# Kernel tuning notes

Measured on AMD Instinct MI355X. Metric: run time of the kernel, lower is better.

## Reference

```python
import jax, jax.numpy as jnp
import numpy as np
import math

B, N, IN_DIM, OUT_DIM, H = 8, 1024, 256, 256, 8
D_K = OUT_DIM // H


def setup_inputs() -> dict:
    key = jax.random.key(0)
    ks = jax.random.split(key, 12)
    s_in = 1.0 / math.sqrt(IN_DIM)
    s_out = 1.0 / math.sqrt(OUT_DIM)
    return {
        "X": jax.random.normal(ks[0], (B, N, IN_DIM), jnp.float32),
        "A": jax.random.randint(ks[1], (B, N, N), 0, 2, jnp.int32),
        "D": jax.random.uniform(ks[2], (B, N, N), jnp.float32),
        "W_q": jax.random.uniform(ks[3], (IN_DIM, OUT_DIM), jnp.float32, -s_in, s_in),
        "b_q": jax.random.uniform(ks[4], (OUT_DIM,), jnp.float32, -s_in, s_in),
        "W_k": jax.random.uniform(ks[5], (IN_DIM, OUT_DIM), jnp.float32, -s_in, s_in),
        "b_k": jax.random.uniform(ks[6], (OUT_DIM,), jnp.float32, -s_in, s_in),
        "W_v": jax.random.uniform(ks[7], (IN_DIM, OUT_DIM), jnp.float32, -s_in, s_in),
        "b_v": jax.random.uniform(ks[8], (OUT_DIM,), jnp.float32, -s_in, s_in),
        "W_o": jax.random.uniform(ks[9], (OUT_DIM, OUT_DIM), jnp.float32, -s_out, s_out),
        "b_o": jax.random.uniform(ks[10], (OUT_DIM,), jnp.float32, -s_out, s_out),
        "dist_scale": jnp.array(1.0, jnp.float32),
    }


def reference(X, A, D, W_q, b_q, W_k, b_k, W_v, b_v, W_o, b_o, dist_scale):
    b, n, _ = X.shape
    # Projections -> [B, H, N, d_k]
    Q = (X @ W_q + b_q).reshape(b, n, H, D_K).transpose(0, 2, 1, 3)
    K = (X @ W_k + b_k).reshape(b, n, H, D_K).transpose(0, 2, 1, 3)
    V = (X @ W_v + b_v).reshape(b, n, H, D_K).transpose(0, 2, 1, 3)
    scores = jnp.einsum("bhqd,bhkd->bhqk", Q, K) / jnp.sqrt(jnp.float32(D_K))
    scores = scores - dist_scale * D[:, None, :, :]
    scores = jnp.where(A[:, None, :, :] <= 0, jnp.float32(-1e9), scores)
    attn = jax.nn.softmax(scores, axis=-1)  # dropout is identity in eval mode
    out = jnp.einsum("bhqk,bhkd->bhqd", attn, V)
    out = out.transpose(0, 2, 1, 3).reshape(b, n, H * D_K)
    return out @ W_o + b_o
```

## Files before the change

kernel.cpp:

```cpp
#include <hip/hip_runtime.h>


typedef _Float16 f16x8 __attribute__((ext_vector_type(8)));
typedef __fp16 h16x2 __attribute__((ext_vector_type(2)));
typedef float f32x4 __attribute__((ext_vector_type(4)));
typedef int i32x4 __attribute__((ext_vector_type(4)));
typedef unsigned short u16x8 __attribute__((ext_vector_type(8)));

#define DEV static __device__ __forceinline__

#define LOG2E 1.4426950408889634f
#define QSCALE 0.2550351062f

DEV unsigned short f2h(float f) {
  _Float16 h = (_Float16)f;
  unsigned short u;
  __builtin_memcpy(&u, &h, 2);
  return u;
}

DEV f32x4 mfma16h(f16x8 a, f16x8 b, f32x4 c) {
  return __builtin_amdgcn_mfma_f32_16x16x32_f16(a, b, c, 0, 0, 0);
}

DEV f16x8 ldfragh(const unsigned short* p) {
  return *reinterpret_cast<const f16x8*>(p);
}

__global__ __launch_bounds__(256) void k_prep_xw(
    const float* __restrict__ X,
    const float* __restrict__ Wq, const float* __restrict__ Wk,
    const float* __restrict__ Wv, const float* __restrict__ Wo,
    unsigned short* __restrict__ Xh, unsigned short* __restrict__ Wt) {
  const int tid = blockIdx.x * 256 + threadIdx.x;
  const int NX4 = (8192 * 256) / 4;
  if (tid < NX4) {
    float4 v = reinterpret_cast<const float4*>(X)[tid];
    union { h16x2 h2[2]; ushort4 u; } o;
    o.h2[0] = __builtin_amdgcn_cvt_pkrtz(v.x, v.y);
    o.h2[1] = __builtin_amdgcn_cvt_pkrtz(v.z, v.w);
    reinterpret_cast<ushort4*>(Xh)[tid] = o.u;
  } else {
    int t = tid - NX4;
    int mat = t >> 16;
    int e = t & 65535;
    int n = e >> 8, k = e & 255;
    const float* W = (mat == 0) ? Wq : (mat == 1) ? Wk : (mat == 2) ? Wv : Wo;
    Wt[t] = f2h(W[k * 256 + n]);
  }
}

__global__ __launch_bounds__(256, 2) void k_qkv_bias(
    const unsigned short* __restrict__ Xh, const unsigned short* __restrict__ Wt,
    const float* __restrict__ bq, const float* __restrict__ bk,
    const float* __restrict__ bv,
    const int* __restrict__ A, const float* __restrict__ D,
    const float* __restrict__ dscale,
    unsigned short* __restrict__ Qb, unsigned short* __restrict__ Kb,
    unsigned short* __restrict__ Vt, unsigned short* __restrict__ Bias) {
  if (blockIdx.x >= 384) {
    const int t = (blockIdx.x - 384) * 256 + threadIdx.x;
    const i32x4 a4 = reinterpret_cast<const i32x4*>(A)[t];
    const f32x4 d4 = reinterpret_cast<const f32x4*>(D)[t];
    const float c = -dscale[0] * LOG2E;
    ushort4 o;
    unsigned short* op = (unsigned short*)&o;
    #pragma unroll
    for (int i = 0; i < 4; ++i)
      op[i] = f2h(a4[i] <= 0 ? -60000.0f : c * d4[i]);
    reinterpret_cast<ushort4*>(Bias)[t] = o;
    return;
  }

  const int lane = threadIdx.x & 63;
  const int w = threadIdx.x >> 6;
  const int lr = lane & 15, lg = lane >> 4;
  const int yy = blockIdx.x >> 5;
  const int mat = yy >> 2;
  const int nloc = (yy & 3) * 64 + w * 16;
  const int mbase = (blockIdx.x & 31) << 8;

  const unsigned short* Wm = Wt + mat * 65536;
  const float* bias = (mat == 0) ? bq : (mat == 1) ? bk : bv;

  f16x8 bfr[8];
  #pragma unroll
  for (int ks = 0; ks < 8; ++ks)
    bfr[ks] = ldfragh(Wm + (nloc + lr) * 256 + ks * 32 + lg * 8);
  const float bb = bias[nloc + lr];
  const int cm = nloc + lr;
  const int hh = cm >> 5, d = cm & 31;

  for (int mt = 0; mt < 16; ++mt) {
    const int m0 = mbase + mt * 16;
    f16x8 a[8];
    #pragma unroll
    for (int ks = 0; ks < 8; ++ks)
      a[ks] = ldfragh(Xh + (m0 + lr) * 256 + ks * 32 + lg * 8);
    f32x4 acc = {0.f, 0.f, 0.f, 0.f};
    #pragma unroll
    for (int ks = 0; ks < 8; ++ks)
      acc = mfma16h(a[ks], bfr[ks], acc);

    if (mat == 2) {
      union { h16x2 h2[2]; ushort4 u; } vv;
      vv.h2[0] = __builtin_amdgcn_cvt_pkrtz(acc[0] + bb, acc[1] + bb);
      vv.h2[1] = __builtin_amdgcn_cvt_pkrtz(acc[2] + bb, acc[3] + bb);
      const int row = m0 + lg * 4;
      const int bidx = row >> 10, nn = row & 1023;
      *reinterpret_cast<ushort4*>(&Vt[(((bidx * 8 + hh) * 32) + d) * 1024 + nn]) = vv.u;
    } else if (mat == 0) {
      #pragma unroll
      for (int i = 0; i < 4; ++i) {
        const int row = m0 + lg * 4 + i;
        const int bidx = row >> 10, nn = row & 1023;
        Qb[(((bidx * 8 + hh) * 1024) + nn) * 32 + d] = f2h((acc[i] + bb) * QSCALE);
      }
    } else {
      #pragma unroll
      for (int i = 0; i < 4; ++i) {
        const int row = m0 + lg * 4 + i;
        const int bidx = row >> 10, nn = row & 1023;
        Kb[(((bidx * 8 + hh) * 1024) + nn) * 32 + d] = f2h(acc[i] + bb);
      }
    }
  }
}

__global__ __launch_bounds__(512, 2) void k_attn(
    const unsigned short* __restrict__ Qb, const unsigned short* __restrict__ Kb,
    const unsigned short* __restrict__ Vt, const unsigned short* __restrict__ Bias,
    unsigned short* __restrict__ AO) {
  __shared__ alignas(16) unsigned short Klds[1024 * 32];
  __shared__ alignas(16) unsigned short Vlds[32 * 1024];
  __shared__ alignas(16) unsigned short Sbuf[8][2][16][40];

  const int tid = threadIdx.x;
  const int lane = tid & 63;
  const int w = tid >> 6;
  const int lr = lane & 15, lg = lane >> 4;
  const int bi = blockIdx.x;
  const int b = bi & 7;
  const int j = bi >> 3;
  const int h = j >> 2, qq = j & 3;
  const int q0w = qq * 256 + w * 32;

  const unsigned short* Kg = Kb + ((size_t)(b * 8 + h) << 15);
  const unsigned short* Vg = Vt + ((size_t)(b * 8 + h) << 15);
  const unsigned short* Qh = Qb + ((size_t)(b * 8 + h) << 15);

  #pragma unroll
  for (int p = 0; p < 8; ++p) {
    const int c = tid + p * 512;
    const int row = c >> 2, seg = c & 3;
    const u16x8 v = *reinterpret_cast<const u16x8*>(Kg + c * 8);
    *reinterpret_cast<u16x8*>(&Klds[row * 32 + ((seg ^ (row & 3)) << 3)]) = v;
  }
  #pragma unroll
  for (int p = 0; p < 8; ++p) {
    const int c = tid + p * 512;
    const int row = c >> 7, ch = c & 127;
    const u16x8 v = *reinterpret_cast<const u16x8*>(Vg + c * 8);
    *reinterpret_cast<u16x8*>(&Vlds[row * 1024 + ((ch ^ (row & 7)) << 3)]) = v;
  }

  f16x8 qf[2];
  qf[0] = ldfragh(Qh + (q0w + lr) * 32 + lg * 8);
  qf[1] = ldfragh(Qh + (q0w + 16 + lr) * 32 + lg * 8);
  const unsigned short* Br0 = Bias + ((size_t)b << 20) + (size_t)(q0w + lr) * 1024;
  const unsigned short* Br1 = Br0 + (size_t)16 * 1024;

  u16x8 bc[2][2], bn[2][2];
  #pragma unroll
  for (int hf = 0; hf < 2; ++hf) {
    bc[0][hf] = *reinterpret_cast<const u16x8*>(Br0 + hf * 32 + lg * 8);
    bc[1][hf] = *reinterpret_cast<const u16x8*>(Br1 + hf * 32 + lg * 8);
  }

  __syncthreads();

  f32x4 o[2][2];
  f32x4 lacc[2];
  #pragma unroll
  for (int s = 0; s < 2; ++s) {
    #pragma unroll
    for (int dh = 0; dh < 2; ++dh) o[s][dh] = f32x4{0.f, 0.f, 0.f, 0.f};
    lacc[s] = f32x4{0.f, 0.f, 0.f, 0.f};
  }
  f16x8 onesv;
  #pragma unroll
  for (int i = 0; i < 8; ++i) onesv[i] = (_Float16)1.0f;

  for (int t = 0; t < 16; ++t) {
    const int k0 = t << 6;
    if (t < 15) {
      #pragma unroll
      for (int hf = 0; hf < 2; ++hf) {
        bn[0][hf] = *reinterpret_cast<const u16x8*>(Br0 + k0 + 64 + hf * 32 + lg * 8);
        bn[1][hf] = *reinterpret_cast<const u16x8*>(Br1 + k0 + 64 + hf * 32 + lg * 8);
      }
    }

    f16x8 kf[4];
    #pragma unroll
    for (int st = 0; st < 4; ++st) {
      const int row = k0 + st * 16 + lr;
      kf[st] = *reinterpret_cast<const f16x8*>(
          &Klds[row * 32 + ((lg ^ (lr & 3)) << 3)]);
    }
    f16x8 vf[2][2];
    #pragma unroll
    for (int dh = 0; dh < 2; ++dh)
      #pragma unroll
      for (int hf = 0; hf < 2; ++hf) {
        const int row = dh * 16 + lr;
        const int ch = t * 8 + ((hf * 4 + lg) ^ (lr & 7));
        vf[dh][hf] = *reinterpret_cast<const f16x8*>(&Vlds[row * 1024 + ch * 8]);
      }

    #pragma unroll
    for (int hf = 0; hf < 2; ++hf) {
      const f32x4 zz = {0.f, 0.f, 0.f, 0.f};
      f32x4 sv[2][2];
      #pragma unroll
      for (int s = 0; s < 2; ++s)
        #pragma unroll
        for (int st = 0; st < 2; ++st)
          sv[s][st] = mfma16h(kf[hf * 2 + st], qf[s], zz);

      #pragma unroll
      for (int s = 0; s < 2; ++s)
        #pragma unroll
        for (int st = 0; st < 2; ++st) {
          union { h16x2 h2[2]; ushort4 u; } sw;
          sw.h2[0] = __builtin_amdgcn_cvt_pkrtz(sv[s][st][0], sv[s][st][1]);
          sw.h2[1] = __builtin_amdgcn_cvt_pkrtz(sv[s][st][2], sv[s][st][3]);
          *reinterpret_cast<ushort4*>(&Sbuf[w][s][lr][st * 16 + lg * 4]) = sw.u;
        }

      #pragma unroll
      for (int s = 0; s < 2; ++s) {
        const f16x8 sf = *reinterpret_cast<const f16x8*>(&Sbuf[w][s][lr][lg * 8]);
        const f16x8 bfv = *reinterpret_cast<const f16x8*>(&bc[s][hf]);
        const f16x8 sb = sf + bfv;
        float e[8];
        #pragma unroll
        for (int i = 0; i < 8; ++i) e[i] = exp2f((float)sb[i]);
        union { h16x2 h2[4]; f16x8 v; } pfu;
        #pragma unroll
        for (int i = 0; i < 4; ++i)
          pfu.h2[i] = __builtin_amdgcn_cvt_pkrtz(e[2 * i], e[2 * i + 1]);
        const f16x8 pf = pfu.v;
        o[s][0] = mfma16h(vf[0][hf], pf, o[s][0]);
        o[s][1] = mfma16h(vf[1][hf], pf, o[s][1]);
        lacc[s] = mfma16h(onesv, pf, lacc[s]);
      }
    }

    #pragma unroll
    for (int s = 0; s < 2; ++s)
      #pragma unroll
      for (int hf = 0; hf < 2; ++hf)
        bc[s][hf] = bn[s][hf];
  }

  #pragma unroll
  for (int s = 0; s < 2; ++s) {
    const float linv = 1.0f / lacc[s][0];
    ushort4 r0, r1;
    unsigned short* r0p = (unsigned short*)&r0;
    unsigned short* r1p = (unsigned short*)&r1;
    #pragma unroll
    for (int i = 0; i < 4; ++i) {
      r0p[i] = f2h(o[s][0][i] * linv);
      r1p[i] = f2h(o[s][1][i] * linv);
    }
    const int row = (b << 10) + q0w + s * 16 + lr;
    *reinterpret_cast<ushort4*>(&AO[row * 256 + h * 32 + lg * 4]) = r0;
    *reinterpret_cast<ushort4*>(&AO[row * 256 + h * 32 + 16 + lg * 4]) = r1;
  }
}

__global__ __launch_bounds__(256, 2) void k_oproj(
    const unsigned short* __restrict__ AO, const unsigned short* __restrict__ Wto,
    const float* __restrict__ bo, float* __restrict__ out) {
  const int lane = threadIdx.x & 63;
  const int w = threadIdx.x >> 6;
  const int lr = lane & 15, lg = lane >> 4;
  const int c0 = blockIdx.y * 64 + w * 16;
  const int mbase = blockIdx.x << 7;

  f16x8 bfr[8];
  #pragma unroll
  for (int ks = 0; ks < 8; ++ks)
    bfr[ks] = ldfragh(Wto + (c0 + lr) * 256 + ks * 32 + lg * 8);
  const float bb = bo[c0 + lr];

  for (int mt = 0; mt < 8; ++mt) {
    const int m0 = mbase + mt * 16;
    f16x8 a[8];
    #pragma unroll
    for (int ks = 0; ks < 8; ++ks)
      a[ks] = ldfragh(AO + (m0 + lr) * 256 + ks * 32 + lg * 8);
    f32x4 acc = {0.f, 0.f, 0.f, 0.f};
    #pragma unroll
    for (int ks = 0; ks < 8; ++ks)
      acc = mfma16h(a[ks], bfr[ks], acc);
    #pragma unroll
    for (int i = 0; i < 4; ++i) {
      const int row = m0 + lg * 4 + i;
      out[row * 256 + c0 + lr] = acc[i] + bb;
    }
  }
}

extern "C" void kernel_launch(void* const* d_in, const int* in_sizes, int n_in,
                              void* d_out, int out_size, void* d_ws, size_t ws_size,
                              hipStream_t stream) {
  const float* X   = (const float*)d_in[0];
  const int*   A   = (const int*)d_in[1];
  const float* D   = (const float*)d_in[2];
  const float* Wq  = (const float*)d_in[3];
  const float* bq  = (const float*)d_in[4];
  const float* Wk  = (const float*)d_in[5];
  const float* bk  = (const float*)d_in[6];
  const float* Wv  = (const float*)d_in[7];
  const float* bv  = (const float*)d_in[8];
  const float* Wo  = (const float*)d_in[9];
  const float* bo  = (const float*)d_in[10];
  const float* dsc = (const float*)d_in[11];
  float* out = (float*)d_out;

  unsigned short* ws = (unsigned short*)d_ws;
  unsigned short* Xh   = ws;
  unsigned short* Wt   = ws + 2097152;
  unsigned short* Qb   = ws + 2359296;
  unsigned short* Kb   = ws + 4456448;
  unsigned short* Vt   = ws + 6553600;
  unsigned short* Bias = ws + 8650752;
  unsigned short* AO   = Xh;

  hipLaunchKernelGGL(k_prep_xw, dim3(3072), dim3(256), 0, stream,
                     X, Wq, Wk, Wv, Wo, Xh, Wt);
  hipLaunchKernelGGL(k_qkv_bias, dim3(8576), dim3(256), 0, stream,
                     Xh, Wt, bq, bk, bv, A, D, dsc, Qb, Kb, Vt, Bias);
  hipLaunchKernelGGL(k_attn, dim3(256), dim3(512), 0, stream,
                     Qb, Kb, Vt, Bias, AO);
  hipLaunchKernelGGL(k_oproj, dim3(64, 4), dim3(256), 0, stream,
                     AO, Wt + 196608, bo, out);
}
```

Baseline: 84.80 us.

## Fuse adjacency mask and distance bias into attention kernel, drop bias precompute

New measurement: 120.7 us. 1.42x slower.

```diff
diff --git a/kernel.cpp b/kernel.cpp
--- a/kernel.cpp
+++ b/kernel.cpp
@@ -50,28 +50,12 @@
   }
 }
 
-__global__ __launch_bounds__(256, 2) void k_qkv_bias(
+__global__ __launch_bounds__(256, 2) void k_qkv(
     const unsigned short* __restrict__ Xh, const unsigned short* __restrict__ Wt,
     const float* __restrict__ bq, const float* __restrict__ bk,
     const float* __restrict__ bv,
-    const int* __restrict__ A, const float* __restrict__ D,
-    const float* __restrict__ dscale,
     unsigned short* __restrict__ Qb, unsigned short* __restrict__ Kb,
-    unsigned short* __restrict__ Vt, unsigned short* __restrict__ Bias) {
-  if (blockIdx.x >= 384) {
-    const int t = (blockIdx.x - 384) * 256 + threadIdx.x;
-    const i32x4 a4 = reinterpret_cast<const i32x4*>(A)[t];
-    const f32x4 d4 = reinterpret_cast<const f32x4*>(D)[t];
-    const float c = -dscale[0] * LOG2E;
-    ushort4 o;
-    unsigned short* op = (unsigned short*)&o;
-    #pragma unroll
-    for (int i = 0; i < 4; ++i)
-      op[i] = f2h(a4[i] <= 0 ? -60000.0f : c * d4[i]);
-    reinterpret_cast<ushort4*>(Bias)[t] = o;
-    return;
-  }
-
+    unsigned short* __restrict__ Vt) {
   const int lane = threadIdx.x & 63;
   const int w = threadIdx.x >> 6;
   const int lr = lane & 15, lg = lane >> 4;
@@ -129,7 +113,8 @@
 
 __global__ __launch_bounds__(512, 2) void k_attn(
     const unsigned short* __restrict__ Qb, const unsigned short* __restrict__ Kb,
-    const unsigned short* __restrict__ Vt, const unsigned short* __restrict__ Bias,
+    const unsigned short* __restrict__ Vt, const int* __restrict__ A,
+    const float* __restrict__ D, const float* __restrict__ dsc,
     unsigned short* __restrict__ AO) {
   __shared__ alignas(16) unsigned short Klds[1024 * 32];
   __shared__ alignas(16) unsigned short Vlds[32 * 1024];
@@ -144,6 +129,7 @@
   const int j = bi >> 3;
   const int h = j >> 2, qq = j & 3;
   const int q0w = qq * 256 + w * 32;
+  const float c = -dsc[0] * LOG2E;
 
   const unsigned short* Kg = Kb + ((size_t)(b * 8 + h) << 15);
   const unsigned short* Vg = Vt + ((size_t)(b * 8 + h) << 15);
@@ -151,31 +137,28 @@
 
   #pragma unroll
   for (int p = 0; p < 8; ++p) {
-    const int c = tid + p * 512;
-    const int row = c >> 2, seg = c & 3;
-    const u16x8 v = *reinterpret_cast<const u16x8*>(Kg + c * 8);
+    const int cc = tid + p * 512;
+    const int row = cc >> 2, seg = cc & 3;
+    const u16x8 v = *reinterpret_cast<const u16x8*>(Kg + cc * 8);
     *reinterpret_cast<u16x8*>(&Klds[row * 32 + ((seg ^ (row & 3)) << 3)]) = v;
   }
   #pragma unroll
   for (int p = 0; p < 8; ++p) {
-    const int c = tid + p * 512;
-    const int row = c >> 7, ch = c & 127;
-    const u16x8 v = *reinterpret_cast<const u16x8*>(Vg + c * 8);
+    const int cc = tid + p * 512;
+    const int row = cc >> 7, ch = cc & 127;
+    const u16x8 v = *reinterpret_cast<const u16x8*>(Vg + cc * 8);
     *reinterpret_cast<u16x8*>(&Vlds[row * 1024 + ((ch ^ (row & 7)) << 3)]) = v;
   }
 
   f16x8 qf[2];
   qf[0] = ldfragh(Qh + (q0w + lr) * 32 + lg * 8);
   qf[1] = ldfragh(Qh + (q0w + 16 + lr) * 32 + lg * 8);
-  const unsigned short* Br0 = Bias + ((size_t)b << 20) + (size_t)(q0w + lr) * 1024;
-  const unsigned short* Br1 = Br0 + (size_t)16 * 1024;
-
-  u16x8 bc[2][2], bn[2][2];
-  #pragma unroll
-  for (int hf = 0; hf < 2; ++hf) {
-    bc[0][hf] = *reinterpret_cast<const u16x8*>(Br0 + hf * 32 + lg * 8);
-    bc[1][hf] = *reinterpret_cast<const u16x8*>(Br1 + hf * 32 + lg * 8);
-  }
+  const int* Ar[2];
+  const float* Dr[2];
+  Ar[0] = A + ((size_t)b << 20) + (size_t)(q0w + lr) * 1024;
+  Ar[1] = Ar[0] + 16 * 1024;
+  Dr[0] = D + ((size_t)b << 20) + (size_t)(q0w + lr) * 1024;
+  Dr[1] = Dr[0] + 16 * 1024;
 
   __syncthreads();
 
@@ -193,13 +176,18 @@
 
   for (int t = 0; t < 16; ++t) {
     const int k0 = t << 6;
-    if (t < 15) {
-      #pragma unroll
-      for (int hf = 0; hf < 2; ++hf) {
-        bn[0][hf] = *reinterpret_cast<const u16x8*>(Br0 + k0 + 64 + hf * 32 + lg * 8);
-        bn[1][hf] = *reinterpret_cast<const u16x8*>(Br1 + k0 + 64 + hf * 32 + lg * 8);
-      }
-    }
+
+    i32x4 ac[2][2][2];
+    f32x4 dc[2][2][2];
+    #pragma unroll
+    for (int s = 0; s < 2; ++s)
+      #pragma unroll
+      for (int hf = 0; hf < 2; ++hf)
+        #pragma unroll
+        for (int jj = 0; jj < 2; ++jj) {
+          ac[s][hf][jj] = *reinterpret_cast<const i32x4*>(Ar[s] + k0 + hf * 32 + lg * 8 + jj * 4);
+          dc[s][hf][jj] = *reinterpret_cast<const f32x4*>(Dr[s] + k0 + hf * 32 + lg * 8 + jj * 4);
+        }
 
     f16x8 kf[4];
     #pragma unroll
@@ -241,11 +229,14 @@
       #pragma unroll
       for (int s = 0; s < 2; ++s) {
         const f16x8 sf = *reinterpret_cast<const f16x8*>(&Sbuf[w][s][lr][lg * 8]);
-        const f16x8 bfv = *reinterpret_cast<const f16x8*>(&bc[s][hf]);
-        const f16x8 sb = sf + bfv;
+        const i32x4 a0 = ac[s][hf][0], a1 = ac[s][hf][1];
+        const f32x4 d0 = dc[s][hf][0], d1 = dc[s][hf][1];
         float e[8];
         #pragma unroll
-        for (int i = 0; i < 8; ++i) e[i] = exp2f((float)sb[i]);
+        for (int i = 0; i < 4; ++i) {
+          e[i]     = (a0[i] <= 0) ? 0.f : exp2f((float)sf[i]     + c * d0[i]);
+          e[i + 4] = (a1[i] <= 0) ? 0.f : exp2f((float)sf[i + 4] + c * d1[i]);
+        }
         union { h16x2 h2[4]; f16x8 v; } pfu;
         #pragma unroll
         for (int i = 0; i < 4; ++i)
@@ -256,12 +247,6 @@
         lacc[s] = mfma16h(onesv, pf, lacc[s]);
       }
     }
-
-    #pragma unroll
-    for (int s = 0; s < 2; ++s)
-      #pragma unroll
-      for (int hf = 0; hf < 2; ++hf)
-        bc[s][hf] = bn[s][hf];
   }
 
   #pragma unroll
@@ -337,15 +322,14 @@
   unsigned short* Qb   = ws + 2359296;
   unsigned short* Kb   = ws + 4456448;
   unsigned short* Vt   = ws + 6553600;
-  unsigned short* Bias = ws + 8650752;
   unsigned short* AO   = Xh;
 
   hipLaunchKernelGGL(k_prep_xw, dim3(3072), dim3(256), 0, stream,
                      X, Wq, Wk, Wv, Wo, Xh, Wt);
-  hipLaunchKernelGGL(k_qkv_bias, dim3(8576), dim3(256), 0, stream,
-                     Xh, Wt, bq, bk, bv, A, D, dsc, Qb, Kb, Vt, Bias);
+  hipLaunchKernelGGL(k_qkv, dim3(384), dim3(256), 0, stream,
+                     Xh, Wt, bq, bk, bv, Qb, Kb, Vt);
   hipLaunchKernelGGL(k_attn, dim3(256), dim3(512), 0, stream,
-                     Qb, Kb, Vt, Bias, AO);
+                     Qb, Kb, Vt, A, D, dsc, AO);
   hipLaunchKernelGGL(k_oproj, dim3(64, 4), dim3(256), 0, stream,
                      AO, Wt + 196608, bo, out);
 }
```
